# Performance work log

Measured on AMD Instinct MI355X. Metric: run time of the kernel, lower is better.

Reference implementation:

```python
import jax, jax.numpy as jnp
import numpy as np

NHID = 1024
HEADS = 16
SEQ = 2048
BATCH = 4


def gelu_bert(x):
    # paper variant: x * sigmoid(1.702 * x)
    return x * jax.nn.sigmoid(1.702 * x)


def setup_inputs() -> dict:
    key = jax.random.key(0)
    ks = jax.random.split(key, 20)
    s = 0.02
    inp = {
        "query": jax.random.normal(ks[0], (SEQ, BATCH, NHID), jnp.float32),
        "key": jax.random.normal(ks[1], (SEQ, BATCH, NHID), jnp.float32),
        "value": jax.random.normal(ks[2], (SEQ, BATCH, NHID), jnp.float32),
        # gating params (torch init is zeros/ones; randomize mildly for a nontrivial baseline)
        "qs_p": jax.random.normal(ks[3], (1, 1, NHID), jnp.float32) * s,
        "ks_p": jax.random.normal(ks[4], (1, 1, NHID), jnp.float32) * s,
        "vs_p": jax.random.normal(ks[5], (1, 1, NHID), jnp.float32) * s,
        # Overparam (vq): Linear(nhid, 2*nhid)
        "vq_w": jax.random.normal(ks[6], (2 * NHID, NHID), jnp.float32) * s,
        "vq_b": jax.random.normal(ks[7], (2 * NHID,), jnp.float32) * s,
        # q/k/v projections: Linear(nhid, nhid)
        "q_w": jax.random.normal(ks[8], (NHID, NHID), jnp.float32) * s,
        "q_b": jax.random.normal(ks[9], (NHID,), jnp.float32) * s,
        "k_w": jax.random.normal(ks[10], (NHID, NHID), jnp.float32) * s,
        "k_b": jax.random.normal(ks[11], (NHID,), jnp.float32) * s,
        "v_w": jax.random.normal(ks[12], (NHID, NHID), jnp.float32) * s,
        "v_b": jax.random.normal(ks[13], (NHID,), jnp.float32) * s,
        # residual gate: Linear(2*nhid, nhid)
        "r_w": jax.random.normal(ks[14], (NHID, 2 * NHID), jnp.float32) * s,
        "r_b": jax.random.normal(ks[15], (NHID,), jnp.float32) * s,
        "r_gate": jnp.ones((1, 1, NHID), jnp.float32),
    }
    return inp


def reference(query, key, value, qs_p, ks_p, vs_p, vq_w, vq_b,
              q_w, q_b, k_w, k_b, v_w, v_b, r_w, r_b, r_gate):
    dim = NHID // HEADS
    # sigmoid gates
    qs = jax.nn.sigmoid(qs_p)
    ksg = jax.nn.sigmoid(ks_p)
    vs0 = jax.nn.sigmoid(vs_p)
    # Overparam on vs: l1 -> split -> sigmoid(f) * tanh(c)
    cf = vs0 @ vq_w.T + vq_b           # [1,1,2*nhid]
    c, f = cf[..., :NHID], cf[..., NHID:]
    vs = jax.nn.sigmoid(f) * jnp.tanh(c)
    # linear projections
    query = query @ q_w.T + q_b
    key = key @ k_w.T + k_b
    value = value @ v_w.T + v_b
    # gated scaling
    q = qs * query                      # [S,B,nhid]
    k = ksg * key
    v = vs * value
    original_q = q
    # to batch-first, then split heads -> [B,H,S,d]
    def split_heads(x):
        x = jnp.transpose(x, (1, 0, 2))                 # [B,S,nhid]
        x = x.reshape(BATCH, -1, HEADS, dim)
        return jnp.transpose(x, (0, 2, 1, 3))           # [B,H,S,d]
    qh, kh, vh = split_heads(q), split_heads(k), split_heads(v)
    scores = jnp.einsum('bhqd,bhkd->bhqk', qh, kh) / jnp.sqrt(jnp.float32(dim))
    weights = jax.nn.softmax(scores, axis=-1)           # [B,H,Sq,Sk]
    mix = jnp.einsum('bhqk,bhkd->bhqd', weights, vh)    # [B,H,S,d]
    mix = jnp.transpose(mix, (0, 2, 1, 3)).reshape(BATCH, -1, NHID)  # [B,S,nhid]
    mix = jnp.transpose(mix, (1, 0, 2))                 # [S,B,nhid]
    # residual gate MLP
    rcat = jnp.concatenate([mix, original_q], axis=-1)  # [S,B,2*nhid]
    r = gelu_bert(rcat @ r_w.T + r_b)
    out = jax.nn.sigmoid(r_gate) * mix + r
    return out
```

## Files before the change

### kernel.cpp

```cpp
#include <hip/hip_runtime.h>
#include <hip/hip_bf16.h>
#include <math.h>

#define SEQ   2048
#define BATCH 4
#define NHID  1024
#define HEADS 16
#define DIM   64
#define MROWS (SEQ*BATCH)
#define LOG2E 1.44269504f

typedef __attribute__((ext_vector_type(8)))  short bf16x8;
typedef __attribute__((ext_vector_type(4)))  float f32x4;
typedef __attribute__((ext_vector_type(16))) float f32x16;

__device__ __forceinline__ float sigf(float x) { return 1.0f / (1.0f + expf(-x)); }

__device__ __forceinline__ unsigned short f2b(float x) {
    unsigned int u = __float_as_uint(x);
    return (unsigned short)((u + 0x7FFFu + ((u >> 16) & 1u)) >> 16);
}
__device__ __forceinline__ float b2f(unsigned short h) {
    return __uint_as_float(((unsigned int)h) << 16);
}
__device__ __forceinline__ unsigned pk2(float lo, float hi) {
    __hip_bfloat162 h = __float22bfloat162_rn(make_float2(lo, hi));
    union { __hip_bfloat162 h; unsigned u; } cv; cv.h = h;
    return cv.u;
}
__device__ __forceinline__ float fexp2(float x) {
    float tf = __builtin_fmaf(x, 8388608.0f, 1065103216.0f);
    return __uint_as_float((unsigned)(int)tf);
}
__device__ __forceinline__ void gload_lds16(const void* g, void* l) {
    __builtin_amdgcn_global_load_lds((const __attribute__((address_space(1))) void*)g,
                                     (__attribute__((address_space(3))) void*)l,
                                     16, 0, 0);
}

__global__ __launch_bounds__(256) void k_prep(const float* __restrict__ vs_p,
                                              const float* __restrict__ vq_w,
                                              const float* __restrict__ vq_b,
                                              float* __restrict__ cf,
                                              const float* __restrict__ s0,
                                              const float* __restrict__ s1,
                                              const float* __restrict__ s2,
                                              const float* __restrict__ s3,
                                              unsigned short* __restrict__ d0,
                                              unsigned short* __restrict__ d1,
                                              unsigned short* __restrict__ d2,
                                              unsigned short* __restrict__ d3)
{
    if (blockIdx.x < 512) {
        const int wave = threadIdx.x >> 6, lane = threadIdx.x & 63;
        const int j = blockIdx.x * 4 + wave;
        const float* w = vq_w + (size_t)j * NHID;
        float p = 0.f;
        for (int i = lane; i < NHID; i += 64) p += sigf(vs_p[i]) * w[i];
#pragma unroll
        for (int off = 32; off; off >>= 1) p += __shfl_down(p, off);
        if (lane == 0) cf[j] = p + vq_b[j];
        return;
    }
    int blk = blockIdx.x - 512;
    const float* src; unsigned short* dst;
    if      (blk < 1024) { src = s0; dst = d0; }
    else if (blk < 2048) { src = s1; dst = d1; blk -= 1024; }
    else if (blk < 3072) { src = s2; dst = d2; blk -= 2048; }
    else                 { src = s3; dst = d3; blk -= 3072; }
    const int i = (blk * 256 + threadIdx.x) * 4;
    float4 v = *(const float4*)(src + i);
    unsigned long long pack = (unsigned long long)f2b(v.x)
                            | ((unsigned long long)f2b(v.y) << 16)
                            | ((unsigned long long)f2b(v.z) << 32)
                            | ((unsigned long long)f2b(v.w) << 48);
    *(unsigned long long*)(dst + i) = pack;
}

__global__ __launch_bounds__(256) void k_scales(const float* __restrict__ qs_p,
                                                const float* __restrict__ ks_p,
                                                const float* __restrict__ r_gate,
                                                const float* __restrict__ cf,
                                                float* __restrict__ sq, float* __restrict__ sk,
                                                float* __restrict__ sv, float* __restrict__ rg)
{
    for (int n = threadIdx.x; n < NHID; n += 256) {
        sq[n] = sigf(qs_p[n]);
        sk[n] = sigf(ks_p[n]) * (0.125f * LOG2E);
        rg[n] = sigf(r_gate[n]);
        sv[n] = sigf(cf[n + NHID]) * tanhf(cf[n]);
    }
}

__global__ __launch_bounds__(256) void k_proj3(const float* __restrict__ A0,
                                               const float* __restrict__ A1,
                                               const float* __restrict__ A2,
                                               const unsigned short* __restrict__ W0,
                                               const unsigned short* __restrict__ W1,
                                               const unsigned short* __restrict__ W2,
                                               const float* __restrict__ b0,
                                               const float* __restrict__ b1,
                                               const float* __restrict__ b2,
                                               const float* __restrict__ c0,
                                               const float* __restrict__ c1,
                                               const float* __restrict__ c2,
                                               unsigned short* __restrict__ o0,
                                               unsigned short* __restrict__ o1,
                                               unsigned short* __restrict__ o2)
{
    __shared__ float          Asf[2][128 * 32];
    __shared__ unsigned short Bs[2][128 * 32];
    const int t = threadIdx.x;
    const int wid = t >> 6, lane = t & 63;
    const int wr = wid >> 1, wc = wid & 1;
    const int f = blockIdx.x;
    const int wg = (f & 7) * 192 + (f >> 3);
    const int seg = wg / 512, inner = wg - seg * 512;
    const int bm = inner >> 3, bn = inner & 7;
    const float* A = seg == 0 ? A0 : seg == 1 ? A1 : A2;
    const unsigned short* W = seg == 0 ? W0 : seg == 1 ? W1 : W2;
    const float* bias  = seg == 0 ? b0 : seg == 1 ? b1 : b2;
    const float* scale = seg == 0 ? c0 : seg == 1 ? c1 : c2;
    unsigned short* outb = seg == 0 ? o0 : seg == 1 ? o1 : o2;
    const float* Ab = A + (size_t)bm * 128 * NHID;
    const unsigned short* Bb = W + (size_t)bn * 128 * NHID;

    f32x4 acc[4][4] = {};

#define PSTAGE(BUF, K0) do {                                                     \
    _Pragma("unroll")                                                            \
    for (int it_ = 0; it_ < 4; ++it_) {                                          \
        const int c_   = it_ * 256 + t;                                          \
        const int row_ = c_ >> 3;                                                \
        const int g_   = (c_ & 7) ^ (row_ & 7);                                  \
        gload_lds16(Ab + (size_t)row_ * NHID + (K0) + g_ * 4,                    \
                    (char*)&Asf[BUF][0] + c_ * 16);                              \
    }                                                                            \
    _Pragma("unroll")                                                            \
    for (int it_ = 0; it_ < 2; ++it_) {                                          \
        const int c_   = it_ * 256 + t;                                          \
        const int row_ = c_ >> 2;                                                \
        const int g_   = (c_ & 3) ^ ((row_ >> 1) & 3);                           \
        gload_lds16(Bb + (size_t)row_ * NHID + (K0) + g_ * 8,                    \
                    (char*)&Bs[BUF][0] + c_ * 16);                               \
    }                                                                            \
} while (0)

#define PCOMP(BUF) do {                                                          \
    bf16x8 af[4], bf[4];                                                         \
    _Pragma("unroll")                                                            \
    for (int mi = 0; mi < 4; ++mi) {                                             \
        const int r   = wr * 64 + mi * 16 + (lane & 15);                         \
        const int gc0 = (lane >> 4) * 2;                                         \
        const int cl0 = gc0 ^ (r & 7);                                           \
        const int cl1 = (gc0 + 1) ^ (r & 7);                                     \
        f32x4 v0 = *(const f32x4*)&Asf[BUF][r * 32 + cl0 * 4];                   \
        f32x4 v1 = *(const f32x4*)&Asf[BUF][r * 32 + cl1 * 4];                   \
        union { unsigned w[4]; bf16x8 v; } pa;                                   \
        pa.w[0] = pk2(v0[0], v0[1]); pa.w[1] = pk2(v0[2], v0[3]);                \
        pa.w[2] = pk2(v1[0], v1[1]); pa.w[3] = pk2(v1[2], v1[3]);                \
        af[mi] = pa.v;                                                           \
    }                                                                            \
    _Pragma("unroll")                                                            \
    for (int ni = 0; ni < 4; ++ni) {                                             \
        const int r  = wc * 64 + ni * 16 + (lane & 15);                          \
        const int cl = (lane >> 4) ^ ((r >> 1) & 3);                             \
        bf[ni] = *(const bf16x8*)&Bs[BUF][r * 32 + cl * 8];                      \
    }                                                                            \
    _Pragma("unroll")                                                            \
    for (int mi = 0; mi < 4; ++mi)                                               \
        _Pragma("unroll")                                                        \
        for (int ni = 0; ni < 4; ++ni)                                           \
            acc[mi][ni] = __builtin_amdgcn_mfma_f32_16x16x32_bf16(af[mi], bf[ni], acc[mi][ni], 0, 0, 0); \
} while (0)

    PSTAGE(0, 0);
#pragma unroll 1
    for (int k0 = 0; k0 < NHID; k0 += 64) {
        __syncthreads();
        if (k0 + 32 < NHID) PSTAGE(1, k0 + 32);
        PCOMP(0);
        __syncthreads();
        if (k0 + 64 < NHID) PSTAGE(0, k0 + 64);
        PCOMP(1);
    }

#pragma unroll
    for (int mi = 0; mi < 4; ++mi) {
#pragma unroll
        for (int r = 0; r < 4; ++r) {
            const int m = bm * 128 + wr * 64 + mi * 16 + (lane >> 4) * 4 + r;
#pragma unroll
            for (int ni = 0; ni < 4; ++ni) {
                const int n = bn * 128 + wc * 64 + ni * 16 + (lane & 15);
                const float v = scale[n] * (acc[mi][ni][r] + bias[n]);
                if (seg == 0) {
                    outb[(size_t)m * 2048 + 1024 + n] = f2b(v);
                } else {
                    const int s = m >> 2, b = m & 3, h = n >> 6, d = n & 63;
                    outb[((size_t)(b * HEADS + h) * SEQ + s) * DIM + d] = f2b(v);
                }
            }
        }
    }
#undef PSTAGE
#undef PCOMP
}

__global__ __launch_bounds__(256) void k_final(const unsigned short* __restrict__ A,
                                               const unsigned short* __restrict__ W,
                                               const float* __restrict__ bias,
                                               const float* __restrict__ rg,
                                               float* __restrict__ outf,
                                               const unsigned short* __restrict__ mixb)
{
    __shared__ unsigned short As[128 * 64];
    __shared__ unsigned short Bs[128 * 64];
    const int t = threadIdx.x;
    const int wid = t >> 6, lane = t & 63;
    const int wr = wid >> 1, wc = wid & 1;
    int wg = blockIdx.y * 64 + blockIdx.x;
    wg = (wg & 7) * 64 + (wg >> 3);
    const int bm = wg >> 3, bn = wg & 7;
    const int K = 2 * NHID;
    const unsigned short* Ab = A + (size_t)bm * 128 * K;
    const unsigned short* Bb = W + (size_t)bn * 128 * K;

    f32x4 acc[4][4] = {};
    for (int k0 = 0; k0 < K; k0 += 64) {
        __syncthreads();
#pragma unroll
        for (int it = 0; it < 4; ++it) {
            const int c   = it * 256 + t;
            const int row = c >> 3;
            const int g8  = (c & 7) ^ (row & 7);
            gload_lds16(Ab + (size_t)row * K + k0 + g8 * 8, (char*)As + c * 16);
            gload_lds16(Bb + (size_t)row * K + k0 + g8 * 8, (char*)Bs + c * 16);
        }
        __syncthreads();
#pragma unroll
        for (int ks = 0; ks < 2; ++ks) {
            bf16x8 af[4], bf[4];
#pragma unroll
            for (int mi = 0; mi < 4; ++mi) {
                const int r  = wr * 64 + mi * 16 + (lane & 15);
                const int c8 = (ks * 4 + (lane >> 4)) ^ (r & 7);
                af[mi] = *(const bf16x8*)&As[r * 64 + c8 * 8];
            }
#pragma unroll
            for (int ni = 0; ni < 4; ++ni) {
                const int r  = wc * 64 + ni * 16 + (lane & 15);
                const int c8 = (ks * 4 + (lane >> 4)) ^ (r & 7);
                bf[ni] = *(const bf16x8*)&Bs[r * 64 + c8 * 8];
            }
#pragma unroll
            for (int mi = 0; mi < 4; ++mi)
#pragma unroll
                for (int ni = 0; ni < 4; ++ni)
                    acc[mi][ni] = __builtin_amdgcn_mfma_f32_16x16x32_bf16(af[mi], bf[ni], acc[mi][ni], 0, 0, 0);
        }
    }

#pragma unroll
    for (int mi = 0; mi < 4; ++mi) {
#pragma unroll
        for (int r = 0; r < 4; ++r) {
            const int m = bm * 128 + wr * 64 + mi * 16 + (lane >> 4) * 4 + r;
#pragma unroll
            for (int ni = 0; ni < 4; ++ni) {
                const int n = bn * 128 + wc * 64 + ni * 16 + (lane & 15);
                const float pre = acc[mi][ni][r] + bias[n];
                const float g = pre * sigf(1.702f * pre);
                const float mx = b2f(mixb[(size_t)m * 2048 + n]);
                outf[(size_t)m * NHID + n] = rg[n] * mx + g;
            }
        }
    }
}

__global__ __launch_bounds__(256) void k_vt(const unsigned short* __restrict__ Vin,
                                            unsigned short* __restrict__ Vout)
{
    __shared__ unsigned short Ls[64][66];
    const int bh = blockIdx.x >> 5, st = blockIdx.x & 31;
    const int t = threadIdx.x;
    const unsigned short* src = Vin + ((size_t)bh * SEQ + st * 64) * DIM;
    {
        const int s = t >> 2, d0 = (t & 3) * 16;
        *(bf16x8*)&Ls[s][d0]     = *(const bf16x8*)&src[s * DIM + d0];
        *(bf16x8*)&Ls[s][d0 + 8] = *(const bf16x8*)&src[s * DIM + d0 + 8];
    }
    __syncthreads();
    const int d = t >> 2, s0 = (t & 3) * 16;
    union { unsigned short h[16]; unsigned long long q[4]; } r;
#pragma unroll
    for (int i = 0; i < 16; ++i) r.h[i] = Ls[s0 + i][d];
    unsigned short* dst = Vout + ((size_t)bh * DIM + d) * SEQ + st * 64 + s0;
    *(unsigned long long*)&dst[0]  = r.q[0];
    *(unsigned long long*)&dst[8]  = r.q[1];
    *(unsigned long long*)&dst[4]  = r.q[2];
    *(unsigned long long*)&dst[12] = r.q[3];
}

#define LDS8(BASE, ROW, C8) \
    (*(const bf16x8*)&(BASE)[((ROW) << 6) + ((((C8) ^ ((ROW) & 7))) << 3)])

#define STAGE(KB, VB, J0) do {                                                   \
    _Pragma("unroll")                                                            \
    for (int it_ = 0; it_ < 2; ++it_) {                                          \
        const int ch_  = it_ * 256 + t;                                          \
        const int row_ = ch_ >> 3;                                               \
        const int c8_  = (ch_ & 7) ^ (row_ & 7);                                 \
        gload_lds16(Kbh + (size_t)((J0) + row_) * DIM + c8_ * 8,                 \
                    (char*)(KB) + ch_ * 16);                                     \
        gload_lds16(Vbh + (size_t)row_ * SEQ + (J0) + c8_ * 8,                   \
                    (char*)(VB) + ch_ * 16);                                     \
    }                                                                            \
} while (0)

#define TILE(KB, VB) do {                                                        \
    f32x16 sA = {}, sB = {};                                                     \
    __builtin_amdgcn_s_setprio(1);                                               \
    _Pragma("unroll")                                                            \
    for (int ds_ = 0; ds_ < 4; ++ds_) {                                          \
        bf16x8 kf0 = LDS8(KB, q31,      ds_ * 2 + g2);                           \
        bf16x8 kf1 = LDS8(KB, 32 + q31, ds_ * 2 + g2);                           \
        sA = __builtin_amdgcn_mfma_f32_32x32x16_bf16(kf0, qf[ds_], sA, 0, 0, 0); \
        sB = __builtin_amdgcn_mfma_f32_32x32x16_bf16(kf1, qf[ds_], sB, 0, 0, 0); \
    }                                                                            \
    __builtin_amdgcn_s_setprio(0);                                               \
    unsigned ppk[16];                                                            \
    _Pragma("unroll")                                                            \
    for (int p = 0; p < 8; ++p) {                                                \
        ppk[p]     = pk2(fexp2(sA[2 * p]), fexp2(sA[2 * p + 1]));                \
        ppk[8 + p] = pk2(fexp2(sB[2 * p]), fexp2(sB[2 * p + 1]));                \
    }                                                                            \
    f32x16 accP = {};                                                            \
    __builtin_amdgcn_s_setprio(1);                                               \
    _Pragma("unroll")                                                            \
    for (int kc = 0; kc < 4; ++kc) {                                             \
        union { unsigned w[4]; bf16x8 v; } up;                                   \
        up.w[0] = ppk[4 * kc + 0];                                               \
        up.w[1] = ppk[4 * kc + 1];                                               \
        up.w[2] = ppk[4 * kc + 2];                                               \
        up.w[3] = ppk[4 * kc + 3];                                               \
        bf16x8 vf0 = LDS8(VB, q31,      kc * 2 + g2);                            \
        bf16x8 vf1 = LDS8(VB, 32 + q31, kc * 2 + g2);                            \
        accP  = __builtin_amdgcn_mfma_f32_32x32x16_bf16(aone.v, up.v, accP, 0, 0, 0);\
        accO0 = __builtin_amdgcn_mfma_f32_32x32x16_bf16(vf0, up.v, accO0, 0, 0, 0);\
        accO1 = __builtin_amdgcn_mfma_f32_32x32x16_bf16(vf1, up.v, accO1, 0, 0, 0);\
    }                                                                            \
    __builtin_amdgcn_s_setprio(0);                                               \
    l_r += accP[0];                                                              \
} while (0)

__global__ __launch_bounds__(256, 4) void k_attn(const unsigned short* __restrict__ Qc,
                                                 const unsigned short* __restrict__ Kb,
                                                 const unsigned short* __restrict__ Vt,
                                                 unsigned short* __restrict__ mixo)
{
    __shared__ unsigned short Ks0[4096], Ks1[4096];
    __shared__ unsigned short Vs0[4096], Vs1[4096];
    const int t = threadIdx.x, wid = t >> 6, l = t & 63;
    const int g2 = l >> 5, q31 = l & 31;
    const int f = blockIdx.x;
    const int bh = (f & 7) + ((f >> 7) << 3);
    const int qt = (f >> 3) & 15;
    const int b = bh >> 4, h = bh & 15;
    const int s_q = qt * 128 + wid * 32 + q31;

    const unsigned short* Kbh = Kb + (size_t)bh * SEQ * DIM;
    const unsigned short* Vbh = Vt + (size_t)bh * DIM * SEQ;
    const unsigned short* Qrow = Qc + (size_t)(s_q * 4 + b) * 2048 + 1024 + h * 64;

    bf16x8 qf[4];
#pragma unroll
    for (int ds_ = 0; ds_ < 4; ++ds_)
        qf[ds_] = *(const bf16x8*)&Qrow[ds_ * 16 + g2 * 8];

    union { unsigned w[4]; bf16x8 v; } aone;
    aone.w[0] = aone.w[1] = aone.w[2] = aone.w[3] = 0x3F803F80u;

    f32x16 accO0 = {}, accO1 = {};
    float l_r = 0.f;

    STAGE(Ks0, Vs0, 0);
#pragma unroll 1
    for (int j0 = 0; j0 < SEQ; j0 += 128) {
        __syncthreads();
        if (j0 + 64 < SEQ) STAGE(Ks1, Vs1, j0 + 64);
        TILE(Ks0, Vs0);
        __syncthreads();
        if (j0 + 128 < SEQ) STAGE(Ks0, Vs0, j0 + 128);
        TILE(Ks1, Vs1);
    }

    const float inv = 1.f / l_r;
    unsigned short* dst = mixo + (size_t)(s_q * 4 + b) * 2048 + h * 64;
#pragma unroll
    for (int reg = 0; reg < 16; reg += 2) {
        const int d0a = (reg & 3) + 8 * (reg >> 2) + 4 * g2;
        *(unsigned*)&dst[d0a]      = pk2(accO0[reg] * inv, accO0[reg + 1] * inv);
        *(unsigned*)&dst[32 + d0a] = pk2(accO1[reg] * inv, accO1[reg + 1] * inv);
    }
}

extern "C" void kernel_launch(void* const* d_in, const int* in_sizes, int n_in,
                              void* d_out, int out_size, void* d_ws, size_t ws_size,
                              hipStream_t stream)
{
    (void)in_sizes; (void)n_in; (void)out_size; (void)ws_size;
    const float* query  = (const float*)d_in[0];
    const float* key    = (const float*)d_in[1];
    const float* value  = (const float*)d_in[2];
    const float* qs_p   = (const float*)d_in[3];
    const float* ks_p   = (const float*)d_in[4];
    const float* vs_p   = (const float*)d_in[5];
    const float* vq_w   = (const float*)d_in[6];
    const float* vq_b   = (const float*)d_in[7];
    const float* q_w    = (const float*)d_in[8];
    const float* q_b    = (const float*)d_in[9];
    const float* k_w    = (const float*)d_in[10];
    const float* k_b    = (const float*)d_in[11];
    const float* v_w    = (const float*)d_in[12];
    const float* v_b    = (const float*)d_in[13];
    const float* r_w    = (const float*)d_in[14];
    const float* r_b    = (const float*)d_in[15];
    const float* r_gate = (const float*)d_in[16];

    float* fws = (float*)d_ws;
    float* sq = fws;
    float* sk = fws + 1024;
    float* sv = fws + 2048;
    float* rg = fws + 3072;
    float* cf = fws + 4096;

    unsigned short* uws = (unsigned short*)(fws + 8192);
    unsigned short* Wq = uws;
    unsigned short* Wk = Wq + (size_t)NHID * NHID;
    unsigned short* Wv = Wk + (size_t)NHID * NHID;
    unsigned short* Wr = Wv + (size_t)NHID * NHID;
    unsigned short* Qc = Wr + (size_t)NHID * 2 * NHID;
    unsigned short* Kb = Qc + (size_t)MROWS * 2 * NHID;
    unsigned short* Vb = Kb + (size_t)BATCH * HEADS * SEQ * DIM;
    unsigned short* Vtmp = Vb + (size_t)BATCH * HEADS * SEQ * DIM;

    k_prep<<<dim3(5632), dim3(256), 0, stream>>>(vs_p, vq_w, vq_b, cf,
                                                 q_w, k_w, v_w, r_w,
                                                 Wq, Wk, Wv, Wr);
    k_scales<<<dim3(1), dim3(256), 0, stream>>>(qs_p, ks_p, r_gate, cf, sq, sk, sv, rg);

    k_proj3<<<dim3(1536), dim3(256), 0, stream>>>(query, key, value, Wq, Wk, Wv,
                                                  q_b, k_b, v_b, sq, sk, sv,
                                                  Qc, Kb, Vtmp);
    k_vt<<<dim3(2048), dim3(256), 0, stream>>>(Vtmp, Vb);

    k_attn<<<dim3(1024), dim3(256), 0, stream>>>(Qc, Kb, Vb, Qc);

    k_final<<<dim3(64, 8), dim3(256), 0, stream>>>(Qc, Wr, r_b, rg, (float*)d_out, Qc);
}
```

Measured before the change: 253.5 us.

## Fuse V transpose into projection epilogue via LDS staging

The V projection segment now writes its tile into shared memory and emits the transposed [B,H,D,S] layout directly from the GEMM epilogue, removing the separate transpose kernel and its intermediate buffer round-trip. Shared memory is reshaped into one byte array so the staging buffers can be reused for the transpose. This saves a kernel launch and a full read/write of V, at the cost of extra syncs and LDS traffic in the V blocks' epilogue.

```diff
diff --git a/kernel.cpp b/kernel.cpp
--- a/kernel.cpp
+++ b/kernel.cpp
@@ -108,8 +108,9 @@
                                                unsigned short* __restrict__ o1,
                                                unsigned short* __restrict__ o2)
 {
-    __shared__ float          Asf[2][128 * 32];
-    __shared__ unsigned short Bs[2][128 * 32];
+    __shared__ char smem[49152];
+    float*          Asf = (float*)smem;
+    unsigned short* Bsm = (unsigned short*)(smem + 32768);
     const int t = threadIdx.x;
     const int wid = t >> 6, lane = t & 63;
     const int wr = wid >> 1, wc = wid & 1;
@@ -134,7 +135,7 @@
         const int row_ = c_ >> 3;                                                \
         const int g_   = (c_ & 7) ^ (row_ & 7);                                  \
         gload_lds16(Ab + (size_t)row_ * NHID + (K0) + g_ * 4,                    \
-                    (char*)&Asf[BUF][0] + c_ * 16);                              \
+                    (char*)&Asf[(BUF) * 4096] + c_ * 16);                        \
     }                                                                            \
     _Pragma("unroll")                                                            \
     for (int it_ = 0; it_ < 2; ++it_) {                                          \
@@ -142,7 +143,7 @@
         const int row_ = c_ >> 2;                                                \
         const int g_   = (c_ & 3) ^ ((row_ >> 1) & 3);                           \
         gload_lds16(Bb + (size_t)row_ * NHID + (K0) + g_ * 8,                    \
-                    (char*)&Bs[BUF][0] + c_ * 16);                               \
+                    (char*)&Bsm[(BUF) * 4096] + c_ * 16);                        \
     }                                                                            \
 } while (0)
 
@@ -154,8 +155,8 @@
         const int gc0 = (lane >> 4) * 2;                                         \
         const int cl0 = gc0 ^ (r & 7);                                           \
         const int cl1 = (gc0 + 1) ^ (r & 7);                                     \
-        f32x4 v0 = *(const f32x4*)&Asf[BUF][r * 32 + cl0 * 4];                   \
-        f32x4 v1 = *(const f32x4*)&Asf[BUF][r * 32 + cl1 * 4];                   \
+        f32x4 v0 = *(const f32x4*)&Asf[(BUF) * 4096 + r * 32 + cl0 * 4];         \
+        f32x4 v1 = *(const f32x4*)&Asf[(BUF) * 4096 + r * 32 + cl1 * 4];         \
         union { unsigned w[4]; bf16x8 v; } pa;                                   \
         pa.w[0] = pk2(v0[0], v0[1]); pa.w[1] = pk2(v0[2], v0[3]);                \
         pa.w[2] = pk2(v1[0], v1[1]); pa.w[3] = pk2(v1[2], v1[3]);                \
@@ -165,7 +166,7 @@
     for (int ni = 0; ni < 4; ++ni) {                                             \
         const int r  = wc * 64 + ni * 16 + (lane & 15);                          \
         const int cl = (lane >> 4) ^ ((r >> 1) & 3);                             \
-        bf[ni] = *(const bf16x8*)&Bs[BUF][r * 32 + cl * 8];                      \
+        bf[ni] = *(const bf16x8*)&Bsm[(BUF) * 4096 + r * 32 + cl * 8];           \
     }                                                                            \
     _Pragma("unroll")                                                            \
     for (int mi = 0; mi < 4; ++mi)                                               \
@@ -184,27 +185,64 @@
         if (k0 + 64 < NHID) PSTAGE(0, k0 + 64);
         PCOMP(1);
     }
-
-#pragma unroll
-    for (int mi = 0; mi < 4; ++mi) {
-#pragma unroll
-        for (int r = 0; r < 4; ++r) {
-            const int m = bm * 128 + wr * 64 + mi * 16 + (lane >> 4) * 4 + r;
-#pragma unroll
-            for (int ni = 0; ni < 4; ++ni) {
-                const int n = bn * 128 + wc * 64 + ni * 16 + (lane & 15);
-                const float v = scale[n] * (acc[mi][ni][r] + bias[n]);
-                if (seg == 0) {
-                    outb[(size_t)m * 2048 + 1024 + n] = f2b(v);
-                } else {
-                    const int s = m >> 2, b = m & 3, h = n >> 6, d = n & 63;
-                    outb[((size_t)(b * HEADS + h) * SEQ + s) * DIM + d] = f2b(v);
+#undef PSTAGE
+#undef PCOMP
+
+    if (seg < 2) {
+#pragma unroll
+        for (int mi = 0; mi < 4; ++mi) {
+#pragma unroll
+            for (int r = 0; r < 4; ++r) {
+                const int m = bm * 128 + wr * 64 + mi * 16 + (lane >> 4) * 4 + r;
+#pragma unroll
+                for (int ni = 0; ni < 4; ++ni) {
+                    const int n = bn * 128 + wc * 64 + ni * 16 + (lane & 15);
+                    const float v = scale[n] * (acc[mi][ni][r] + bias[n]);
+                    if (seg == 0) {
+                        outb[(size_t)m * 2048 + 1024 + n] = f2b(v);
+                    } else {
+                        const int s = m >> 2, b = m & 3, h = n >> 6, d = n & 63;
+                        outb[((size_t)(b * HEADS + h) * SEQ + s) * DIM + d] = f2b(v);
+                    }
                 }
             }
         }
-    }
-#undef PSTAGE
-#undef PCOMP
+        return;
+    }
+
+    unsigned short* L = (unsigned short*)smem;
+    __syncthreads();
+#pragma unroll
+    for (int mi = 0; mi < 4; ++mi) {
+#pragma unroll
+        for (int r = 0; r < 4; ++r) {
+            const int ml = wr * 64 + mi * 16 + (lane >> 4) * 4 + r;
+#pragma unroll
+            for (int ni = 0; ni < 4; ++ni) {
+                const int nl = wc * 64 + ni * 16 + (lane & 15);
+                const int n = bn * 128 + nl;
+                L[nl * 130 + ml] = f2b(scale[n] * (acc[mi][ni][r] + bias[n]));
+            }
+        }
+    }
+    __syncthreads();
+    const int hl = t >> 7, d = (t >> 1) & 63, half = t & 1;
+    const int nlr = hl * 64 + d;
+    const int sl0 = half * 16;
+#pragma unroll
+    for (int b = 0; b < 4; ++b) {
+        unsigned short* dst = o2 + ((size_t)((b * HEADS) + 2 * bn + hl) * DIM + d) * SEQ
+                            + bm * 32 + sl0;
+#pragma unroll
+        for (int q = 0; q < 4; ++q) {
+            union { unsigned short h[4]; unsigned long long u; } pk;
+#pragma unroll
+            for (int j = 0; j < 4; ++j)
+                pk.h[j] = L[nlr * 130 + (sl0 + q * 4 + j) * 4 + b];
+            const int po = (q == 1) ? 8 : (q == 2) ? 4 : (q == 3) ? 12 : 0;
+            *(unsigned long long*)&dst[po] = pk.u;
+        }
+    }
 }
 
 __global__ __launch_bounds__(256) void k_final(const unsigned short* __restrict__ A,
@@ -276,30 +314,6 @@
             }
         }
     }
-}
-
-__global__ __launch_bounds__(256) void k_vt(const unsigned short* __restrict__ Vin,
-                                            unsigned short* __restrict__ Vout)
-{
-    __shared__ unsigned short Ls[64][66];
-    const int bh = blockIdx.x >> 5, st = blockIdx.x & 31;
-    const int t = threadIdx.x;
-    const unsigned short* src = Vin + ((size_t)bh * SEQ + st * 64) * DIM;
-    {
-        const int s = t >> 2, d0 = (t & 3) * 16;
-        *(bf16x8*)&Ls[s][d0]     = *(const bf16x8*)&src[s * DIM + d0];
-        *(bf16x8*)&Ls[s][d0 + 8] = *(const bf16x8*)&src[s * DIM + d0 + 8];
-    }
-    __syncthreads();
-    const int d = t >> 2, s0 = (t & 3) * 16;
-    union { unsigned short h[16]; unsigned long long q[4]; } r;
-#pragma unroll
-    for (int i = 0; i < 16; ++i) r.h[i] = Ls[s0 + i][d];
-    unsigned short* dst = Vout + ((size_t)bh * DIM + d) * SEQ + st * 64 + s0;
-    *(unsigned long long*)&dst[0]  = r.q[0];
-    *(unsigned long long*)&dst[8]  = r.q[1];
-    *(unsigned long long*)&dst[4]  = r.q[2];
-    *(unsigned long long*)&dst[12] = r.q[3];
 }
 
 #define LDS8(BASE, ROW, C8) \
@@ -443,7 +457,6 @@
     unsigned short* Qc = Wr + (size_t)NHID * 2 * NHID;
     unsigned short* Kb = Qc + (size_t)MROWS * 2 * NHID;
     unsigned short* Vb = Kb + (size_t)BATCH * HEADS * SEQ * DIM;
-    unsigned short* Vtmp = Vb + (size_t)BATCH * HEADS * SEQ * DIM;
 
     k_prep<<<dim3(5632), dim3(256), 0, stream>>>(vs_p, vq_w, vq_b, cf,
                                                  q_w, k_w, v_w, r_w,
@@ -452,8 +465,7 @@
 
     k_proj3<<<dim3(1536), dim3(256), 0, stream>>>(query, key, value, Wq, Wk, Wv,
                                                   q_b, k_b, v_b, sq, sk, sv,
-                                                  Qc, Kb, Vtmp);
-    k_vt<<<dim3(2048), dim3(256), 0, stream>>>(Vtmp, Vb);
+                                                  Qc, Kb, Vb);
 
     k_attn<<<dim3(1024), dim3(256), 0, stream>>>(Qc, Kb, Vb, Qc);
 
```

Result: no change. 254.5 us (+0.4%).
